# Kernel optimization log

Hardware: AMD Instinct MI355X
Metric: run time of the kernel (lower is better)

The kernel has to match this reference:

```python
import jax, jax.numpy as jnp
import numpy as np

D_MODEL = 1024

def setup_inputs() -> dict:
    key = jax.random.key(0)
    ks = jax.random.split(key, 9)
    D = D_MODEL
    s = 1.0 / np.sqrt(D)
    return {
        "X": jax.random.normal(ks[0], (4, 2048, D), dtype=jnp.float32),
        "Wq": jax.random.uniform(ks[1], (D, D), jnp.float32, -s, s),
        "bq": jax.random.uniform(ks[2], (D,), jnp.float32, -s, s),
        "Wk": jax.random.uniform(ks[3], (D, D), jnp.float32, -s, s),
        "bk": jax.random.uniform(ks[4], (D,), jnp.float32, -s, s),
        "Wv": jax.random.uniform(ks[5], (D, D), jnp.float32, -s, s),
        "bv": jax.random.uniform(ks[6], (D,), jnp.float32, -s, s),
        "Wo": jax.random.uniform(ks[7], (D, D), jnp.float32, -s, s),
        "bo": jax.random.uniform(ks[8], (D,), jnp.float32, -s, s),
    }

def reference(X, Wq, bq, Wk, bk, Wv, bv, Wo, bo):
    B, N, D = X.shape
    # torch nn.Linear: x @ W.T + b
    q = jnp.einsum('bnd,ed->bne', X, Wq) + bq
    k = jnp.einsum('bnd,ed->bne', X, Wk) + bk
    v = jnp.einsum('bnd,ed->bne', X, Wv) + bv
    scores = jnp.einsum('bqd,bkd->bqk', q, k) / jnp.sqrt(jnp.float32(D))
    # faithful to source: tril ones kept as +1.0, zeros -> -inf, added to scores
    tril = jnp.tril(jnp.ones((N, N), dtype=bool))
    mask = jnp.where(tril, jnp.float32(1.0), jnp.float32(-jnp.inf))
    scores = scores + mask
    weights = jax.nn.softmax(scores, axis=-1)
    ctx = jnp.einsum('bqk,bkd->bqd', weights, v)
    return jnp.einsum('bnd,ed->bne', ctx, Wo) + bo
```

## Files before the change

kernel.cpp:

```cpp
#include <hip/hip_runtime.h>
#include <hip/hip_bf16.h>
#include <stdint.h>


typedef __hip_bfloat16 bf16;
typedef short bf16x8v __attribute__((ext_vector_type(8)));
typedef short bf16x4v __attribute__((ext_vector_type(4)));
typedef float f32x4   __attribute__((ext_vector_type(4)));

#define DEV static __device__ __forceinline__

DEV void gload_lds16(const void* g, void* l) {
  __builtin_amdgcn_global_load_lds(
      (const __attribute__((address_space(1))) void*)g,
      (__attribute__((address_space(3))) void*)l, 16u, 0, 0u);
}

struct alignas(8) bf16q { bf16 a, b, c, d; };

__global__ __launch_bounds__(256)
void k_f32_to_bf16(const float* __restrict__ in, bf16* __restrict__ out, long n4) {
  long i = (long)blockIdx.x * blockDim.x + threadIdx.x;
  if (i >= n4) return;
  float4 v = ((const float4*)in)[i];
  bf16q o{__float2bfloat16(v.x), __float2bfloat16(v.y),
          __float2bfloat16(v.z), __float2bfloat16(v.w)};
  ((bf16q*)out)[i] = o;
}

template<bool OUT_BF16, bool HAS_BIAS, int CAUSAL>
__global__ __launch_bounds__(256)
void k_gemm_bt(const bf16* __restrict__ A, const bf16* __restrict__ B,
               const float* __restrict__ bias, void* __restrict__ Cout,
               int M, int N, int K, float scale,
               int lda, int ldb, int ldc,
               long sA, long sB, long sC)
{
  const int tn = blockIdx.x, tm = blockIdx.y, bz = blockIdx.z;
  if (CAUSAL == 1 && tn > tm) return;
  const bf16* Ab = A + (long)bz * sA;
  const bf16* Bb = B + (long)bz * sB;

  __shared__ bf16 As[2][128 * 32];
  __shared__ bf16 Bs[2][128 * 32];

  const int t = threadIdx.x;
  const int lane = t & 63;
  const int w = t >> 6;
  const int wr = w >> 1, wc = w & 1;

  f32x4 acc[4][4] = {};

  const int m0 = tm * 128, n0 = tn * 128;
  const int srow = t >> 2;
  const int scol = (t & 3) * 8;

  int kend = K;
  if (CAUSAL == 2) { int ke = (tm + 1) * 128; kend = ke < K ? ke : K; }
  const int nt = kend >> 5;

  const int fr = lane & 15;
  const int kc = (lane >> 4) * 8;

#pragma unroll
  for (int r = 0; r < 2; ++r) {
    int row = srow + r * 64;
    gload_lds16(Ab + (long)(m0 + row) * lda + scol, &As[0][row * 32 + scol]);
    gload_lds16(Bb + (long)(n0 + row) * ldb + scol, &Bs[0][row * 32 + scol]);
  }
  __syncthreads();

  int cur = 0;
  for (int ts = 0; ts < nt; ++ts) {
    if (ts + 1 < nt) {
      int k0 = (ts + 1) << 5;
#pragma unroll
      for (int r = 0; r < 2; ++r) {
        int row = srow + r * 64;
        gload_lds16(Ab + (long)(m0 + row) * lda + (k0 + scol), &As[cur ^ 1][row * 32 + scol]);
        gload_lds16(Bb + (long)(n0 + row) * ldb + (k0 + scol), &Bs[cur ^ 1][row * 32 + scol]);
      }
    }

    bf16x8v af[4], bf_[4];
#pragma unroll
    for (int i = 0; i < 4; i++)
      af[i] = *(const bf16x8v*)&As[cur][(wr * 64 + i * 16 + fr) * 32 + kc];
#pragma unroll
    for (int j = 0; j < 4; j++)
      bf_[j] = *(const bf16x8v*)&Bs[cur][(wc * 64 + j * 16 + fr) * 32 + kc];

#pragma unroll
    for (int i = 0; i < 4; i++)
#pragma unroll
      for (int j = 0; j < 4; j++)
        acc[i][j] = __builtin_amdgcn_mfma_f32_16x16x32_bf16(af[i], bf_[j], acc[i][j], 0, 0, 0);

    __syncthreads();
    cur ^= 1;
  }

  const int rq = (lane >> 4) * 4;
#pragma unroll
  for (int i = 0; i < 4; i++) {
#pragma unroll
    for (int j = 0; j < 4; j++) {
#pragma unroll
      for (int r = 0; r < 4; r++) {
        int m = m0 + wr * 64 + i * 16 + rq + r;
        int n = n0 + wc * 64 + j * 16 + fr;
        float v = acc[i][j][r] * scale;
        if (HAS_BIAS) v += bias[n];
        if (OUT_BF16)
          ((bf16*)Cout + (long)bz * sC)[(long)m * ldc + n] = __float2bfloat16(v);
        else
          ((float*)Cout + (long)bz * sC)[(long)m * ldc + n] = v;
      }
    }
  }
}

__global__ __launch_bounds__(256)
void k_softmax_causal(const float* __restrict__ S, bf16* __restrict__ P) {
  const long row = blockIdx.x;
  const int q = (int)(row & 2047);
  const int kend = ((q >> 7) + 1) << 7;
  const float* s = S + row * 2048;
  bf16* p = P + row * 2048;
  const int t = threadIdx.x;

  float e[8];
  float m = -3.4e38f;
#pragma unroll
  for (int i = 0; i < 8; i++) {
    int k = t + i * 256;
    float v = -3.4e38f;
    if (k <= q) v = s[k];
    e[i] = v;
    m = fmaxf(m, v);
  }
#pragma unroll
  for (int off = 1; off < 64; off <<= 1) m = fmaxf(m, __shfl_xor(m, off, 64));
  __shared__ float red[8];
  if ((t & 63) == 0) red[t >> 6] = m;
  __syncthreads();
  m = fmaxf(fmaxf(red[0], red[1]), fmaxf(red[2], red[3]));

  float sum = 0.f;
#pragma unroll
  for (int i = 0; i < 8; i++) {
    int k = t + i * 256;
    float x = (k <= q) ? __expf(e[i] - m) : 0.f;
    e[i] = x;
    sum += x;
  }
#pragma unroll
  for (int off = 1; off < 64; off <<= 1) sum += __shfl_xor(sum, off, 64);
  if ((t & 63) == 0) red[4 + (t >> 6)] = sum;
  __syncthreads();
  sum = red[4] + red[5] + red[6] + red[7];
  float inv = 1.f / sum;
#pragma unroll
  for (int i = 0; i < 8; i++) {
    int k = t + i * 256;
    if (k < kend) p[k] = __float2bfloat16(e[i] * inv);
  }
}

__global__ __launch_bounds__(256)
void k_transpose_bf16(const bf16* __restrict__ V, bf16* __restrict__ Vt,
                      int in_ld, int out_ld, long in_bs, long out_bs) {
  __shared__ bf16 tile[64][68];
  const bf16* v = V + (long)blockIdx.z * in_bs;
  bf16* vt = Vt + (long)blockIdx.z * out_bs;
  const int k0 = blockIdx.y * 64;
  const int d0 = blockIdx.x * 64;
  const int t = threadIdx.x;
  const int c4 = (t & 15) * 4;
  const int r = t >> 4;
#pragma unroll
  for (int p2 = 0; p2 < 4; p2++) {
    int row = r + p2 * 16;
    bf16x4v val = *(const bf16x4v*)&v[(long)(k0 + row) * in_ld + d0 + c4];
    *(bf16x4v*)&tile[row][c4] = val;
  }
  __syncthreads();
#pragma unroll
  for (int p2 = 0; p2 < 4; p2++) {
    int drow = r + p2 * 16;
    bf16q o{tile[c4 + 0][drow], tile[c4 + 1][drow],
            tile[c4 + 2][drow], tile[c4 + 3][drow]};
    *(bf16q*)&vt[(long)(d0 + drow) * out_ld + k0 + c4] = o;
  }
}

extern "C" void kernel_launch(void* const* d_in, const int* in_sizes, int n_in,
                              void* d_out, int out_size, void* d_ws, size_t ws_size,
                              hipStream_t stream)
{
  const float* X  = (const float*)d_in[0];
  const float* Wq = (const float*)d_in[1];
  const float* bq = (const float*)d_in[2];
  const float* Wk = (const float*)d_in[3];
  const float* bk = (const float*)d_in[4];
  const float* Wv = (const float*)d_in[5];
  const float* bv = (const float*)d_in[6];
  const float* Wo = (const float*)d_in[7];
  const float* bo = (const float*)d_in[8];

  const long Nt = 2048, D = 1024;
  const long TOK = 4 * Nt;

  char* ws = (char*)d_ws;
  const size_t MB = 1024 * 1024;
  bf16*  QKVb = (bf16*)(ws + 0);
  bf16*  Wcat = (bf16*)(ws + 48 * MB);
  bf16*  Wob  = (bf16*)(ws + 54 * MB);
  float* bcat = (float*)(ws + 56 * MB);
  bf16*  Vt   = (bf16*)(ws + 57 * MB);
  bf16*  Cx   = (bf16*)(ws + 73 * MB);
  bf16*  Pb   = (bf16*)(ws + 89 * MB);
  bf16*  Xb   = (bf16*)(ws + 121 * MB);
  float* Sf   = (float*)(ws + 121 * MB);

  dim3 blk(256);

  k_f32_to_bf16<<<dim3(8192), blk, 0, stream>>>(X,  Xb,  TOK * D / 4);
  k_f32_to_bf16<<<dim3(1024), blk, 0, stream>>>(Wq, Wcat,                Wq ? D * D / 4 : 0);
  k_f32_to_bf16<<<dim3(1024), blk, 0, stream>>>(Wk, Wcat + D * D,        D * D / 4);
  k_f32_to_bf16<<<dim3(1024), blk, 0, stream>>>(Wv, Wcat + 2 * D * D,    D * D / 4);
  k_f32_to_bf16<<<dim3(1024), blk, 0, stream>>>(Wo, Wob,                 D * D / 4);

  hipMemcpyAsync(bcat,        bq, D * 4, hipMemcpyDeviceToDevice, stream);
  hipMemcpyAsync(bcat + D,    bk, D * 4, hipMemcpyDeviceToDevice, stream);
  hipMemcpyAsync(bcat + 2*D,  bv, D * 4, hipMemcpyDeviceToDevice, stream);

  k_gemm_bt<true, true, 0><<<dim3(24, 64, 1), blk, 0, stream>>>(
      Xb, Wcat, bcat, QKVb, 8192, 3072, 1024, 1.f,
      1024, 1024, 3072, 0, 0, 0);

  k_transpose_bf16<<<dim3(16, 32, 4), blk, 0, stream>>>(
      QKVb + 2048, Vt, 3072, 2048, Nt * 3072, D * Nt);

  k_gemm_bt<false, false, 1><<<dim3(16, 16, 4), blk, 0, stream>>>(
      QKVb, QKVb + 1024, nullptr, Sf, 2048, 2048, 1024, 0.03125f,
      3072, 3072, 2048, Nt * 3072, Nt * 3072, Nt * Nt);

  k_softmax_causal<<<dim3(8192), blk, 0, stream>>>(Sf, Pb);

  k_gemm_bt<true, false, 2><<<dim3(8, 16, 4), blk, 0, stream>>>(
      Pb, Vt, nullptr, Cx, 2048, 1024, 2048, 1.f,
      2048, 2048, 1024, Nt * Nt, D * Nt, Nt * D);

  k_gemm_bt<false, true, 0><<<dim3(8, 64, 1), blk, 0, stream>>>(
      Cx, Wob, bo, d_out, 8192, 1024, 1024, 1.f,
      1024, 1024, 1024, 0, 0, 0);
}
```

Baseline: 332.3 us.

## Replace GEMM with 256x256-tile 8-wave kernel using swizzled LDS and interleaved staging

Replaces the 128x128, 4-wave GEMM with a 256x256-tile, 512-thread kernel that uses 128KB of dynamic LDS, a 64-wide K step, XOR-swizzled LDS addressing and a remapped workgroup order that groups tiles in chunks of eight. Global-to-LDS staging is split into half-tiles interleaved between four MFMA phases, with explicit waitcnt and barriers, sched barriers and setprio. The aim is more data reuse per load, fewer LDS bank conflicts and better overlap of memory traffic with MFMA work. The causal softmax block size changes to 256 to match the new tile size. The trade-offs are heavier register and LDS use per block, and fewer blocks in the smaller launches.

```diff
diff --git a/kernel.cpp b/kernel.cpp
--- a/kernel.cpp
+++ b/kernel.cpp
@@ -29,88 +29,146 @@
 }
 
 template<bool OUT_BF16, bool HAS_BIAS, int CAUSAL>
-__global__ __launch_bounds__(256)
-void k_gemm_bt(const bf16* __restrict__ A, const bf16* __restrict__ B,
-               const float* __restrict__ bias, void* __restrict__ Cout,
-               int M, int N, int K, float scale,
-               int lda, int ldb, int ldc,
-               long sA, long sB, long sC)
+__global__ __launch_bounds__(512, 2)
+void k_gemm8(const bf16* __restrict__ A, const bf16* __restrict__ B,
+             const float* __restrict__ bias, void* __restrict__ Cout,
+             int M, int N, int K, float scale,
+             int lda, int ldb, int ldc, long sA, long sB, long sC)
 {
-  const int tn = blockIdx.x, tm = blockIdx.y, bz = blockIdx.z;
+  extern __shared__ char smem[];
+  const int gx = gridDim.x;
+  const int nwg = gx * gridDim.y;
+  const int lin0 = blockIdx.y * gx + blockIdx.x;
+  const int cpx = nwg >> 3;
+  const int lin = (lin0 & 7) * cpx + (lin0 >> 3);
+  const int tn = lin % gx, tm = lin / gx;
+  const int bz = blockIdx.z;
   if (CAUSAL == 1 && tn > tm) return;
+
   const bf16* Ab = A + (long)bz * sA;
   const bf16* Bb = B + (long)bz * sB;
-
-  __shared__ bf16 As[2][128 * 32];
-  __shared__ bf16 Bs[2][128 * 32];
+  const int m0 = tm * 256, n0 = tn * 256;
+
+  int kend = K;
+  if (CAUSAL == 2) { int ke = (tm + 1) * 256; kend = ke < K ? ke : K; }
+  const int nt = kend >> 6;
 
   const int t = threadIdx.x;
   const int lane = t & 63;
   const int w = t >> 6;
-  const int wr = w >> 1, wc = w & 1;
-
-  f32x4 acc[4][4] = {};
-
-  const int m0 = tm * 128, n0 = tn * 128;
-  const int srow = t >> 2;
-  const int scol = (t & 3) * 8;
-
-  int kend = K;
-  if (CAUSAL == 2) { int ke = (tm + 1) * 128; kend = ke < K ? ke : K; }
-  const int nt = kend >> 5;
-
+  const int wr = w >> 2, wc = w & 3;
   const int fr = lane & 15;
-  const int kc = (lane >> 4) * 8;
-
-#pragma unroll
-  for (int r = 0; r < 2; ++r) {
-    int row = srow + r * 64;
-    gload_lds16(Ab + (long)(m0 + row) * lda + scol, &As[0][row * 32 + scol]);
-    gload_lds16(Bb + (long)(n0 + row) * ldb + scol, &Bs[0][row * 32 + scol]);
-  }
-  __syncthreads();
-
-  int cur = 0;
-  for (int ts = 0; ts < nt; ++ts) {
-    if (ts + 1 < nt) {
-      int k0 = (ts + 1) << 5;
-#pragma unroll
-      for (int r = 0; r < 2; ++r) {
-        int row = srow + r * 64;
-        gload_lds16(Ab + (long)(m0 + row) * lda + (k0 + scol), &As[cur ^ 1][row * 32 + scol]);
-        gload_lds16(Bb + (long)(n0 + row) * ldb + (k0 + scol), &Bs[cur ^ 1][row * 32 + scol]);
+  const int kq = lane >> 4;
+
+  auto stage = [&](int isB, int h, int tt) {
+    const bf16* src = isB ? Bb : Ab;
+    const int ld = isB ? ldb : lda;
+    const int b0_ = isB ? n0 : m0;
+    char* dst = smem + (tt & 1) * 65536 + isB * 32768 + h * 16384;
+    const int k0 = tt << 6;
+#pragma unroll
+    for (int j = 0; j < 2; ++j) {
+      int lin16 = (t + j * 512) * 16;
+      int lg = lin16 ^ (((lin16 >> 9) & 3) << 5);
+      int row = lg >> 7;
+      int el = (lg & 127) >> 1;
+      gload_lds16(src + (long)(b0_ + h * 128 + row) * ld + (k0 + el),
+                  dst + lin16);
+    }
+  };
+
+  bf16x8v a[4][2], b0f[2][2], b1f[2][2];
+
+  auto ldA = [&](int mh, int buf) {
+    const char* base = smem + buf * 65536 + wr * 16384;
+#pragma unroll
+    for (int i = 0; i < 4; ++i)
+#pragma unroll
+      for (int ks = 0; ks < 2; ++ks) {
+        int r = mh * 64 + i * 16 + fr;
+        int lam = (r * 128 + ks * 64 + kq * 16) ^ (((r >> 2) & 3) << 5);
+        a[i][ks] = *(const bf16x8v*)(base + lam);
       }
-    }
-
-    bf16x8v af[4], bf_[4];
-#pragma unroll
-    for (int i = 0; i < 4; i++)
-      af[i] = *(const bf16x8v*)&As[cur][(wr * 64 + i * 16 + fr) * 32 + kc];
-#pragma unroll
-    for (int j = 0; j < 4; j++)
-      bf_[j] = *(const bf16x8v*)&Bs[cur][(wc * 64 + j * 16 + fr) * 32 + kc];
-
-#pragma unroll
-    for (int i = 0; i < 4; i++)
-#pragma unroll
-      for (int j = 0; j < 4; j++)
-        acc[i][j] = __builtin_amdgcn_mfma_f32_16x16x32_bf16(af[i], bf_[j], acc[i][j], 0, 0, 0);
-
-    __syncthreads();
-    cur ^= 1;
-  }
+  };
+  auto ldB = [&](bf16x8v (&bf_)[2][2], int nh, int buf) {
+    const char* base = smem + buf * 65536 + 32768 + (wc >> 1) * 16384;
+#pragma unroll
+    for (int j = 0; j < 2; ++j)
+#pragma unroll
+      for (int ks = 0; ks < 2; ++ks) {
+        int r = (wc & 1) * 64 + nh * 32 + j * 16 + fr;
+        int lam = (r * 128 + ks * 64 + kq * 16) ^ (((r >> 2) & 3) << 5);
+        bf_[j][ks] = *(const bf16x8v*)(base + lam);
+      }
+  };
+
+  f32x4 acc[8][4] = {};
+
+#define MFMA16(mh, bb, nh)                                                   \
+  _Pragma("unroll") for (int i = 0; i < 4; ++i)                              \
+  _Pragma("unroll") for (int j = 0; j < 2; ++j)                              \
+  _Pragma("unroll") for (int ks = 0; ks < 2; ++ks)                           \
+    acc[(mh)*4 + i][(nh)*2 + j] = __builtin_amdgcn_mfma_f32_16x16x32_bf16(   \
+        a[i][ks], bb[j][ks], acc[(mh)*4 + i][(nh)*2 + j], 0, 0, 0);
+
+  stage(1, 0, 0); stage(0, 0, 0);
+  stage(0, 1, 0); stage(1, 1, 0);
+  stage(1, 0, 1); stage(0, 0, 1);
+
+  for (int G = 0; G < nt; ++G) {
+    const int buf = G & 1;
+    asm volatile("s_waitcnt vmcnt(4)" ::: "memory");
+    __builtin_amdgcn_s_barrier();
+    __builtin_amdgcn_sched_barrier(0);
+
+    ldA(0, buf); ldB(b0f, 0, buf);
+    if (G + 1 < nt) stage(0, 1, G + 1);
+    __builtin_amdgcn_s_barrier();
+    __builtin_amdgcn_sched_barrier(0);
+    __builtin_amdgcn_s_setprio(1);
+    MFMA16(0, b0f, 0);
+    __builtin_amdgcn_s_setprio(0);
+    __builtin_amdgcn_s_barrier();
+
+    ldB(b1f, 1, buf);
+    if (G + 1 < nt) stage(1, 1, G + 1);
+    __builtin_amdgcn_s_barrier();
+    __builtin_amdgcn_sched_barrier(0);
+    __builtin_amdgcn_s_setprio(1);
+    MFMA16(0, b1f, 1);
+    __builtin_amdgcn_s_setprio(0);
+    __builtin_amdgcn_s_barrier();
+
+    ldA(1, buf);
+    if (G + 2 < nt) stage(1, 0, G + 2);
+    __builtin_amdgcn_s_barrier();
+    __builtin_amdgcn_sched_barrier(0);
+    __builtin_amdgcn_s_setprio(1);
+    MFMA16(1, b0f, 0);
+    __builtin_amdgcn_s_setprio(0);
+    __builtin_amdgcn_s_barrier();
+
+    if (G + 2 < nt) stage(0, 0, G + 2);
+    __builtin_amdgcn_s_barrier();
+    __builtin_amdgcn_sched_barrier(0);
+    __builtin_amdgcn_s_setprio(1);
+    MFMA16(1, b1f, 1);
+    __builtin_amdgcn_s_setprio(0);
+    __builtin_amdgcn_s_barrier();
+  }
+#undef MFMA16
 
   const int rq = (lane >> 4) * 4;
 #pragma unroll
-  for (int i = 0; i < 4; i++) {
-#pragma unroll
-    for (int j = 0; j < 4; j++) {
-#pragma unroll
-      for (int r = 0; r < 4; r++) {
-        int m = m0 + wr * 64 + i * 16 + rq + r;
-        int n = n0 + wc * 64 + j * 16 + fr;
-        float v = acc[i][j][r] * scale;
-        if (HAS_BIAS) v += bias[n];
+  for (int nf = 0; nf < 4; ++nf) {
+    const int n = n0 + wc * 64 + nf * 16 + fr;
+    const float bv_ = HAS_BIAS ? bias[n] : 0.f;
+#pragma unroll
+    for (int mf = 0; mf < 8; ++mf) {
+#pragma unroll
+      for (int r = 0; r < 4; ++r) {
+        const int m = m0 + wr * 128 + mf * 16 + rq + r;
+        float v = acc[mf][nf][r] * scale + bv_;
         if (OUT_BF16)
           ((bf16*)Cout + (long)bz * sC)[(long)m * ldc + n] = __float2bfloat16(v);
         else
@@ -124,7 +182,7 @@
 void k_softmax_causal(const float* __restrict__ S, bf16* __restrict__ P) {
   const long row = blockIdx.x;
   const int q = (int)(row & 2047);
-  const int kend = ((q >> 7) + 1) << 7;
+  const int kend = ((q >> 8) + 1) << 8;
   const float* s = S + row * 2048;
   bf16* p = P + row * 2048;
   const int t = threadIdx.x;
@@ -223,36 +281,46 @@
   bf16*  Xb   = (bf16*)(ws + 121 * MB);
   float* Sf   = (float*)(ws + 121 * MB);
 
-  dim3 blk(256);
+  const int SMEM = 131072;
+  hipFuncSetAttribute((const void*)k_gemm8<true,  true,  0>,
+                      hipFuncAttributeMaxDynamicSharedMemorySize, SMEM);
+  hipFuncSetAttribute((const void*)k_gemm8<false, false, 1>,
+                      hipFuncAttributeMaxDynamicSharedMemorySize, SMEM);
+  hipFuncSetAttribute((const void*)k_gemm8<true,  false, 2>,
+                      hipFuncAttributeMaxDynamicSharedMemorySize, SMEM);
+  hipFuncSetAttribute((const void*)k_gemm8<false, true,  0>,
+                      hipFuncAttributeMaxDynamicSharedMemorySize, SMEM);
+
+  dim3 blk(256), blk8(512);
 
   k_f32_to_bf16<<<dim3(8192), blk, 0, stream>>>(X,  Xb,  TOK * D / 4);
-  k_f32_to_bf16<<<dim3(1024), blk, 0, stream>>>(Wq, Wcat,                Wq ? D * D / 4 : 0);
-  k_f32_to_bf16<<<dim3(1024), blk, 0, stream>>>(Wk, Wcat + D * D,        D * D / 4);
-  k_f32_to_bf16<<<dim3(1024), blk, 0, stream>>>(Wv, Wcat + 2 * D * D,    D * D / 4);
-  k_f32_to_bf16<<<dim3(1024), blk, 0, stream>>>(Wo, Wob,                 D * D / 4);
-
-  hipMemcpyAsync(bcat,        bq, D * 4, hipMemcpyDeviceToDevice, stream);
-  hipMemcpyAsync(bcat + D,    bk, D * 4, hipMemcpyDeviceToDevice, stream);
-  hipMemcpyAsync(bcat + 2*D,  bv, D * 4, hipMemcpyDeviceToDevice, stream);
-
-  k_gemm_bt<true, true, 0><<<dim3(24, 64, 1), blk, 0, stream>>>(
+  k_f32_to_bf16<<<dim3(1024), blk, 0, stream>>>(Wq, Wcat,             D * D / 4);
+  k_f32_to_bf16<<<dim3(1024), blk, 0, stream>>>(Wk, Wcat + D * D,     D * D / 4);
+  k_f32_to_bf16<<<dim3(1024), blk, 0, stream>>>(Wv, Wcat + 2 * D * D, D * D / 4);
+  k_f32_to_bf16<<<dim3(1024), blk, 0, stream>>>(Wo, Wob,              D * D / 4);
+
+  hipMemcpyAsync(bcat,       bq, D * 4, hipMemcpyDeviceToDevice, stream);
+  hipMemcpyAsync(bcat + D,   bk, D * 4, hipMemcpyDeviceToDevice, stream);
+  hipMemcpyAsync(bcat + 2*D, bv, D * 4, hipMemcpyDeviceToDevice, stream);
+
+  k_gemm8<true, true, 0><<<dim3(12, 32, 1), blk8, SMEM, stream>>>(
       Xb, Wcat, bcat, QKVb, 8192, 3072, 1024, 1.f,
       1024, 1024, 3072, 0, 0, 0);
 
   k_transpose_bf16<<<dim3(16, 32, 4), blk, 0, stream>>>(
       QKVb + 2048, Vt, 3072, 2048, Nt * 3072, D * Nt);
 
-  k_gemm_bt<false, false, 1><<<dim3(16, 16, 4), blk, 0, stream>>>(
+  k_gemm8<false, false, 1><<<dim3(8, 8, 4), blk8, SMEM, stream>>>(
       QKVb, QKVb + 1024, nullptr, Sf, 2048, 2048, 1024, 0.03125f,
       3072, 3072, 2048, Nt * 3072, Nt * 3072, Nt * Nt);
 
   k_softmax_causal<<<dim3(8192), blk, 0, stream>>>(Sf, Pb);
 
-  k_gemm_bt<true, false, 2><<<dim3(8, 16, 4), blk, 0, stream>>>(
+  k_gemm8<true, false, 2><<<dim3(4, 8, 4), blk8, SMEM, stream>>>(
       Pb, Vt, nullptr, Cx, 2048, 1024, 2048, 1.f,
       2048, 2048, 1024, Nt * Nt, D * Nt, Nt * D);
 
-  k_gemm_bt<false, true, 0><<<dim3(8, 64, 1), blk, 0, stream>>>(
+  k_gemm8<false, true, 0><<<dim3(4, 32, 1), blk8, SMEM, stream>>>(
       Cx, Wob, bo, d_out, 8192, 1024, 1024, 1.f,
       1024, 1024, 1024, 0, 0, 0);
 }
```

Result: slower. 357.6 us (+7.6%).

## Triple-buffer GEMM LDS with XOR swizzle and store scores as bf16

Applied to the files above, without the earlier changes.

The GEMM body moves from a double-buffered LDS pipeline to a three-stage one. It issues prefetches two tiles ahead, waits with explicit vmcnt counts and a single barrier per step, and applies an XOR swizzle to the LDS layout to avoid bank conflicts. The score matrix is written as bf16 rather than f32, which halves score traffic, and the softmax kernel now reads and writes contiguous 8-element vectors. Launch bounds request 3 blocks per CU, and bias loads are hoisted out of the inner epilogue loop. Rounding the scores to bf16 before softmax adds precision loss.

```diff
diff --git a/kernel.cpp b/kernel.cpp
--- a/kernel.cpp
+++ b/kernel.cpp
@@ -29,88 +29,95 @@
 }
 
 template<bool OUT_BF16, bool HAS_BIAS, int CAUSAL>
-__global__ __launch_bounds__(256)
-void k_gemm_bt(const bf16* __restrict__ A, const bf16* __restrict__ B,
-               const float* __restrict__ bias, void* __restrict__ Cout,
-               int M, int N, int K, float scale,
-               int lda, int ldb, int ldc,
-               long sA, long sB, long sC)
+DEV void gemm_body(const bf16* __restrict__ A, const bf16* __restrict__ B,
+                   const float* __restrict__ bias, void* __restrict__ Cout,
+                   int K, float scale, int lda, int ldb, int ldc,
+                   long sA, long sB, long sC)
 {
+  __shared__ char smem[49152];
   const int tn = blockIdx.x, tm = blockIdx.y, bz = blockIdx.z;
   if (CAUSAL == 1 && tn > tm) return;
   const bf16* Ab = A + (long)bz * sA;
   const bf16* Bb = B + (long)bz * sB;
-
-  __shared__ bf16 As[2][128 * 32];
-  __shared__ bf16 Bs[2][128 * 32];
+  const int m0 = tm * 128, n0 = tn * 128;
+
+  int kend = K;
+  if (CAUSAL == 2) { int ke = (tm + 1) * 128; kend = ke < K ? ke : K; }
+  const int nt = kend >> 5;
 
   const int t = threadIdx.x;
   const int lane = t & 63;
   const int w = t >> 6;
   const int wr = w >> 1, wc = w & 1;
+  const int fr = lane & 15;
+  const int kq = lane >> 4;
+
+  auto stage = [&](int tt, int slot) {
+    char* dA = smem + slot * 8192;
+    char* dB = smem + 24576 + slot * 8192;
+    const int k0 = tt << 5;
+#pragma unroll
+    for (int j = 0; j < 2; ++j) {
+      int lin16 = (t + j * 256) * 16;
+      int lg = lin16 ^ (((lin16 >> 6) & 3) << 4);
+      int row = lg >> 6;
+      int el = (lg & 63) >> 1;
+      gload_lds16(Ab + (long)(m0 + row) * lda + (k0 + el), dA + lin16);
+      gload_lds16(Bb + (long)(n0 + row) * ldb + (k0 + el), dB + lin16);
+    }
+  };
 
   f32x4 acc[4][4] = {};
 
-  const int m0 = tm * 128, n0 = tn * 128;
-  const int srow = t >> 2;
-  const int scol = (t & 3) * 8;
-
-  int kend = K;
-  if (CAUSAL == 2) { int ke = (tm + 1) * 128; kend = ke < K ? ke : K; }
-  const int nt = kend >> 5;
-
-  const int fr = lane & 15;
-  const int kc = (lane >> 4) * 8;
-
-#pragma unroll
-  for (int r = 0; r < 2; ++r) {
-    int row = srow + r * 64;
-    gload_lds16(Ab + (long)(m0 + row) * lda + scol, &As[0][row * 32 + scol]);
-    gload_lds16(Bb + (long)(n0 + row) * ldb + scol, &Bs[0][row * 32 + scol]);
-  }
-  __syncthreads();
-
-  int cur = 0;
+  stage(0, 0);
+  stage(1, 1);
+
+  int cur = 0, s2 = 2;
   for (int ts = 0; ts < nt; ++ts) {
-    if (ts + 1 < nt) {
-      int k0 = (ts + 1) << 5;
-#pragma unroll
-      for (int r = 0; r < 2; ++r) {
-        int row = srow + r * 64;
-        gload_lds16(Ab + (long)(m0 + row) * lda + (k0 + scol), &As[cur ^ 1][row * 32 + scol]);
-        gload_lds16(Bb + (long)(n0 + row) * ldb + (k0 + scol), &Bs[cur ^ 1][row * 32 + scol]);
-      }
-    }
-
+    if (ts + 1 < nt) asm volatile("s_waitcnt vmcnt(4)" ::: "memory");
+    else             asm volatile("s_waitcnt vmcnt(0)" ::: "memory");
+    __builtin_amdgcn_s_barrier();
+    __builtin_amdgcn_sched_barrier(0);
+
+    if (ts + 2 < nt) stage(ts + 2, s2);
+
+    const char* As_ = smem + cur * 8192;
+    const char* Bs_ = smem + 24576 + cur * 8192;
     bf16x8v af[4], bf_[4];
 #pragma unroll
-    for (int i = 0; i < 4; i++)
-      af[i] = *(const bf16x8v*)&As[cur][(wr * 64 + i * 16 + fr) * 32 + kc];
-#pragma unroll
-    for (int j = 0; j < 4; j++)
-      bf_[j] = *(const bf16x8v*)&Bs[cur][(wc * 64 + j * 16 + fr) * 32 + kc];
-
-#pragma unroll
-    for (int i = 0; i < 4; i++)
-#pragma unroll
-      for (int j = 0; j < 4; j++)
+    for (int i = 0; i < 4; ++i) {
+      int off = (wr * 64 + i * 16 + fr) * 64 + kq * 16;
+      int lam = off ^ (((off >> 6) & 3) << 4);
+      af[i] = *(const bf16x8v*)(As_ + lam);
+    }
+#pragma unroll
+    for (int j = 0; j < 4; ++j) {
+      int off = (wc * 64 + j * 16 + fr) * 64 + kq * 16;
+      int lam = off ^ (((off >> 6) & 3) << 4);
+      bf_[j] = *(const bf16x8v*)(Bs_ + lam);
+    }
+
+#pragma unroll
+    for (int i = 0; i < 4; ++i)
+#pragma unroll
+      for (int j = 0; j < 4; ++j)
         acc[i][j] = __builtin_amdgcn_mfma_f32_16x16x32_bf16(af[i], bf_[j], acc[i][j], 0, 0, 0);
 
-    __syncthreads();
-    cur ^= 1;
+    cur = (cur == 2) ? 0 : cur + 1;
+    s2  = (s2 == 2) ? 0 : s2 + 1;
   }
 
   const int rq = (lane >> 4) * 4;
 #pragma unroll
-  for (int i = 0; i < 4; i++) {
-#pragma unroll
-    for (int j = 0; j < 4; j++) {
-#pragma unroll
-      for (int r = 0; r < 4; r++) {
-        int m = m0 + wr * 64 + i * 16 + rq + r;
-        int n = n0 + wc * 64 + j * 16 + fr;
-        float v = acc[i][j][r] * scale;
-        if (HAS_BIAS) v += bias[n];
+  for (int i = 0; i < 4; ++i) {
+#pragma unroll
+    for (int j = 0; j < 4; ++j) {
+      const int n = n0 + wc * 64 + j * 16 + fr;
+      const float bv_ = HAS_BIAS ? bias[n] : 0.f;
+#pragma unroll
+      for (int r = 0; r < 4; ++r) {
+        const int m = m0 + wr * 64 + i * 16 + rq + r;
+        float v = acc[i][j][r] * scale + bv_;
         if (OUT_BF16)
           ((bf16*)Cout + (long)bz * sC)[(long)m * ldc + n] = __float2bfloat16(v);
         else
@@ -120,24 +127,48 @@
   }
 }
 
+__global__ __launch_bounds__(256, 3)
+void k_qkv(const bf16* A, const bf16* B, const float* bias, void* C,
+           int K, float scale, int lda, int ldb, int ldc) {
+  gemm_body<true, true, 0>(A, B, bias, C, K, scale, lda, ldb, ldc, 0, 0, 0);
+}
+__global__ __launch_bounds__(256, 3)
+void k_sgemm(const bf16* A, const bf16* B, void* C,
+             int K, float scale, int lda, int ldb, int ldc,
+             long sA, long sB, long sC) {
+  gemm_body<true, false, 1>(A, B, nullptr, C, K, scale, lda, ldb, ldc, sA, sB, sC);
+}
+__global__ __launch_bounds__(256, 3)
+void k_pv(const bf16* A, const bf16* B, void* C,
+          int K, float scale, int lda, int ldb, int ldc,
+          long sA, long sB, long sC) {
+  gemm_body<true, false, 2>(A, B, nullptr, C, K, scale, lda, ldb, ldc, sA, sB, sC);
+}
+__global__ __launch_bounds__(256, 3)
+void k_oproj(const bf16* A, const bf16* B, const float* bias, void* C,
+             int K, float scale, int lda, int ldb, int ldc) {
+  gemm_body<false, true, 0>(A, B, bias, C, K, scale, lda, ldb, ldc, 0, 0, 0);
+}
+
 __global__ __launch_bounds__(256)
-void k_softmax_causal(const float* __restrict__ S, bf16* __restrict__ P) {
+void k_softmax(const bf16* __restrict__ S, bf16* __restrict__ P) {
   const long row = blockIdx.x;
   const int q = (int)(row & 2047);
   const int kend = ((q >> 7) + 1) << 7;
-  const float* s = S + row * 2048;
+  const bf16* s = S + row * 2048;
   bf16* p = P + row * 2048;
   const int t = threadIdx.x;
 
+  bf16x8v v = *(const bf16x8v*)&s[t * 8];
   float e[8];
   float m = -3.4e38f;
 #pragma unroll
   for (int i = 0; i < 8; i++) {
-    int k = t + i * 256;
-    float v = -3.4e38f;
-    if (k <= q) v = s[k];
-    e[i] = v;
-    m = fmaxf(m, v);
+    int k = t * 8 + i;
+    unsigned short u = (unsigned short)v[i];
+    float x = (k <= q) ? __bfloat162float(*(const bf16*)&u) : -3.4e38f;
+    e[i] = x;
+    m = fmaxf(m, x);
   }
 #pragma unroll
   for (int off = 1; off < 64; off <<= 1) m = fmaxf(m, __shfl_xor(m, off, 64));
@@ -149,7 +180,7 @@
   float sum = 0.f;
 #pragma unroll
   for (int i = 0; i < 8; i++) {
-    int k = t + i * 256;
+    int k = t * 8 + i;
     float x = (k <= q) ? __expf(e[i] - m) : 0.f;
     e[i] = x;
     sum += x;
@@ -159,11 +190,16 @@
   if ((t & 63) == 0) red[4 + (t >> 6)] = sum;
   __syncthreads();
   sum = red[4] + red[5] + red[6] + red[7];
-  float inv = 1.f / sum;
-#pragma unroll
-  for (int i = 0; i < 8; i++) {
-    int k = t + i * 256;
-    if (k < kend) p[k] = __float2bfloat16(e[i] * inv);
+  const float inv = 1.f / sum;
+
+  if (t * 8 < kend) {
+    bf16x8v o;
+#pragma unroll
+    for (int i = 0; i < 8; i++) {
+      bf16 b = __float2bfloat16(e[i] * inv);
+      o[i] = *(const short*)&b;
+    }
+    *(bf16x8v*)&p[t * 8] = o;
   }
 }
 
@@ -221,38 +257,36 @@
   bf16*  Cx   = (bf16*)(ws + 73 * MB);
   bf16*  Pb   = (bf16*)(ws + 89 * MB);
   bf16*  Xb   = (bf16*)(ws + 121 * MB);
-  float* Sf   = (float*)(ws + 121 * MB);
+  bf16*  Sb   = (bf16*)(ws + 137 * MB);
 
   dim3 blk(256);
 
   k_f32_to_bf16<<<dim3(8192), blk, 0, stream>>>(X,  Xb,  TOK * D / 4);
-  k_f32_to_bf16<<<dim3(1024), blk, 0, stream>>>(Wq, Wcat,                Wq ? D * D / 4 : 0);
-  k_f32_to_bf16<<<dim3(1024), blk, 0, stream>>>(Wk, Wcat + D * D,        D * D / 4);
-  k_f32_to_bf16<<<dim3(1024), blk, 0, stream>>>(Wv, Wcat + 2 * D * D,    D * D / 4);
-  k_f32_to_bf16<<<dim3(1024), blk, 0, stream>>>(Wo, Wob,                 D * D / 4);
-
-  hipMemcpyAsync(bcat,        bq, D * 4, hipMemcpyDeviceToDevice, stream);
-  hipMemcpyAsync(bcat + D,    bk, D * 4, hipMemcpyDeviceToDevice, stream);
-  hipMemcpyAsync(bcat + 2*D,  bv, D * 4, hipMemcpyDeviceToDevice, stream);
-
-  k_gemm_bt<true, true, 0><<<dim3(24, 64, 1), blk, 0, stream>>>(
-      Xb, Wcat, bcat, QKVb, 8192, 3072, 1024, 1.f,
-      1024, 1024, 3072, 0, 0, 0);
+  k_f32_to_bf16<<<dim3(1024), blk, 0, stream>>>(Wq, Wcat,             D * D / 4);
+  k_f32_to_bf16<<<dim3(1024), blk, 0, stream>>>(Wk, Wcat + D * D,     D * D / 4);
+  k_f32_to_bf16<<<dim3(1024), blk, 0, stream>>>(Wv, Wcat + 2 * D * D, D * D / 4);
+  k_f32_to_bf16<<<dim3(1024), blk, 0, stream>>>(Wo, Wob,              D * D / 4);
+
+  hipMemcpyAsync(bcat,       bq, D * 4, hipMemcpyDeviceToDevice, stream);
+  hipMemcpyAsync(bcat + D,   bk, D * 4, hipMemcpyDeviceToDevice, stream);
+  hipMemcpyAsync(bcat + 2*D, bv, D * 4, hipMemcpyDeviceToDevice, stream);
+
+  k_qkv<<<dim3(24, 64, 1), blk, 0, stream>>>(
+      Xb, Wcat, bcat, QKVb, 1024, 1.f, 1024, 1024, 3072);
 
   k_transpose_bf16<<<dim3(16, 32, 4), blk, 0, stream>>>(
       QKVb + 2048, Vt, 3072, 2048, Nt * 3072, D * Nt);
 
-  k_gemm_bt<false, false, 1><<<dim3(16, 16, 4), blk, 0, stream>>>(
-      QKVb, QKVb + 1024, nullptr, Sf, 2048, 2048, 1024, 0.03125f,
+  k_sgemm<<<dim3(16, 16, 4), blk, 0, stream>>>(
+      QKVb, QKVb + 1024, Sb, 1024, 0.03125f,
       3072, 3072, 2048, Nt * 3072, Nt * 3072, Nt * Nt);
 
-  k_softmax_causal<<<dim3(8192), blk, 0, stream>>>(Sf, Pb);
-
-  k_gemm_bt<true, false, 2><<<dim3(8, 16, 4), blk, 0, stream>>>(
-      Pb, Vt, nullptr, Cx, 2048, 1024, 2048, 1.f,
-      2048, 2048, 1024, Nt * Nt, D * Nt, Nt * D);
-
-  k_gemm_bt<false, true, 0><<<dim3(8, 64, 1), blk, 0, stream>>>(
-      Cx, Wob, bo, d_out, 8192, 1024, 1024, 1.f,
-      1024, 1024, 1024, 0, 0, 0);
-}
+  k_softmax<<<dim3(8192), blk, 0, stream>>>(Sb, Pb);
+
+  k_pv<<<dim3(8, 16, 4), blk, 0, stream>>>(
+      Pb, Vt, Cx, 2048, 1.f, 2048, 2048, 1024,
+      Nt * Nt, D * Nt, Nt * D);
+
+  k_oproj<<<dim3(8, 64, 1), blk, 0, stream>>>(
+      Cx, Wob, bo, d_out, 1024, 1.f, 1024, 1024, 1024);
+}
```

Measured after the change: 311.7 us. 6.2% less time.
